# Kernel tuning notes

Measured on AMD Instinct MI355X. Metric: run time of the kernel, lower is better.

Reference implementation:

```python
import jax, jax.numpy as jnp
import numpy as np

DIM = 64  # scaling dim from __init__


def setup_inputs() -> dict:
    key = jax.random.key(0)
    kq, kk, kv = jax.random.split(key, 3)
    B, N, D = 16, 2048, 64
    Q = jax.random.normal(kq, (B, N, D), dtype=jnp.float32)
    K = jax.random.normal(kk, (B, N, D), dtype=jnp.float32)
    V = jax.random.normal(kv, (B, N, D), dtype=jnp.float32)
    return {"Q": Q, "K": K, "V": V}


def reference(Q, K, V):
    # Original transposes K to [B, d, N]; the E/F Linformer projections are
    # constructed but their application guards are always False, so the math
    # is plain scaled-dot-product attention. Dropout p=0 (eval baseline).
    scale = 1.0 / (DIM ** 0.5)
    QK = jnp.einsum('bnd,bmd->bnm', Q, K) * scale          # [B, N, N]
    attn_weights = jax.nn.softmax(QK, axis=-1)             # [B, N, N]
    out = jnp.einsum('bnm,bmd->bnd', attn_weights, V)      # [B, N, d]
    return out, attn_weights
```

## Files before the change

### kernel.cpp

```cpp
#include <hip/hip_runtime.h>

#define B_  16
#define N_  2048
#define D_  64
#define KT  64
#define NTILES (N_ / KT)
#define SCALE_LOG2 0.18033688011112042f

typedef __attribute__((ext_vector_type(8))) short  frag8;
typedef __attribute__((ext_vector_type(4))) float  floatx4;

__device__ __forceinline__ unsigned short f2bf(float f) {
    unsigned int u = __builtin_bit_cast(unsigned int, f);
    u += 0x7fffu + ((u >> 16) & 1u);
    return (unsigned short)(u >> 16);
}

__global__ __launch_bounds__(256) void attn_fused(
    const float* __restrict__ Q, const float* __restrict__ K,
    const float* __restrict__ V, float* __restrict__ out,
    float* __restrict__ attn)
{
    __shared__ unsigned short Qs[64][72];
    __shared__ unsigned short Ks[64][72];
    __shared__ unsigned short Vt[64][72];
    __shared__ unsigned short Ps[4][16][72];

    const int qtile = blockIdx.x;
    const int b     = blockIdx.y;
    const int qbase = qtile * 64;
    const int tid   = threadIdx.x;
    const int w     = tid >> 6;
    const int lane  = tid & 63;
    const int lm    = lane & 15;
    const int quad  = lane >> 4;
    const int q8    = quad * 8;

    const int srow = tid >> 2;
    const int sc0  = (tid & 3) * 16;
    const int vswz = srow ^ (((sc0 >> 4) & 3) << 3);

    {
        const float4* src = (const float4*)(Q + ((size_t)(b*N_ + qbase + srow))*D_ + sc0);
        #pragma unroll
        for (int i = 0; i < 4; ++i) {
            float4 f = src[i];
            ushort4 u; u.x=f2bf(f.x); u.y=f2bf(f.y); u.z=f2bf(f.z); u.w=f2bf(f.w);
            *(ushort4*)&Qs[srow][sc0 + i*4] = u;
        }
    }
    __syncthreads();
    const frag8 aq0 = *(const frag8*)&Qs[w*16 + lm][q8];
    const frag8 aq1 = *(const frag8*)&Qs[w*16 + lm][32 + q8];

    float s[4] = {0.f, 0.f, 0.f, 0.f};

    ushort4 kreg[4];
    {
        const float4* src = (const float4*)(K + ((size_t)(b*N_ + srow))*D_ + sc0);
        #pragma unroll
        for (int i = 0; i < 4; ++i) {
            float4 f = src[i];
            kreg[i].x=f2bf(f.x); kreg[i].y=f2bf(f.y); kreg[i].z=f2bf(f.z); kreg[i].w=f2bf(f.w);
        }
    }

    for (int t = 0; t < NTILES; ++t) {
        __syncthreads();
        #pragma unroll
        for (int i = 0; i < 4; ++i)
            *(ushort4*)&Ks[srow][sc0 + i*4] = kreg[i];
        __syncthreads();

        float4 fnext[4];
        if (t+1 < NTILES) {
            const float4* src = (const float4*)(K + ((size_t)(b*N_ + (t+1)*KT + srow))*D_ + sc0);
            #pragma unroll
            for (int i = 0; i < 4; ++i) fnext[i] = src[i];
        }

        floatx4 acc[4];
        #pragma unroll
        for (int ns = 0; ns < 4; ++ns) {
            frag8 b0 = *(const frag8*)&Ks[ns*16 + lm][q8];
            frag8 b1 = *(const frag8*)&Ks[ns*16 + lm][32 + q8];
            floatx4 a = {0.f, 0.f, 0.f, 0.f};
            a = __builtin_amdgcn_mfma_f32_16x16x32_bf16(aq0, b0, a, 0, 0, 0);
            a = __builtin_amdgcn_mfma_f32_16x16x32_bf16(aq1, b1, a, 0, 0, 0);
            acc[ns] = a;
        }
        #pragma unroll
        for (int ns = 0; ns < 4; ++ns)
            #pragma unroll
            for (int r = 0; r < 4; ++r)
                s[r] += exp2f(acc[ns][r] * SCALE_LOG2);

        if (t+1 < NTILES) {
            #pragma unroll
            for (int i = 0; i < 4; ++i) {
                kreg[i].x=f2bf(fnext[i].x); kreg[i].y=f2bf(fnext[i].y);
                kreg[i].z=f2bf(fnext[i].z); kreg[i].w=f2bf(fnext[i].w);
            }
        }
    }

    float invl[4];
    #pragma unroll
    for (int r = 0; r < 4; ++r) {
        float v = s[r];
        #pragma unroll
        for (int off = 1; off < 16; off <<= 1)
            v += __shfl_xor(v, off, 64);
        invl[r] = 1.0f / v;
    }

    floatx4 oacc[4];
    #pragma unroll
    for (int ns = 0; ns < 4; ++ns) oacc[ns] = (floatx4){0.f, 0.f, 0.f, 0.f};

    unsigned short vbf[16];
    {
        const float4* srcK = (const float4*)(K + ((size_t)(b*N_ + srow))*D_ + sc0);
        const float4* srcV = (const float4*)(V + ((size_t)(b*N_ + srow))*D_ + sc0);
        #pragma unroll
        for (int i = 0; i < 4; ++i) {
            float4 f = srcK[i];
            kreg[i].x=f2bf(f.x); kreg[i].y=f2bf(f.y); kreg[i].z=f2bf(f.z); kreg[i].w=f2bf(f.w);
        }
        #pragma unroll
        for (int i = 0; i < 4; ++i) {
            float4 f = srcV[i];
            vbf[i*4+0]=f2bf(f.x); vbf[i*4+1]=f2bf(f.y);
            vbf[i*4+2]=f2bf(f.z); vbf[i*4+3]=f2bf(f.w);
        }
    }

    for (int t = 0; t < NTILES; ++t) {
        __syncthreads();
        #pragma unroll
        for (int i = 0; i < 4; ++i)
            *(ushort4*)&Ks[srow][sc0 + i*4] = kreg[i];
        #pragma unroll
        for (int i = 0; i < 4; ++i) {
            Vt[sc0 + i*4 + 0][vswz] = vbf[i*4+0];
            Vt[sc0 + i*4 + 1][vswz] = vbf[i*4+1];
            Vt[sc0 + i*4 + 2][vswz] = vbf[i*4+2];
            Vt[sc0 + i*4 + 3][vswz] = vbf[i*4+3];
        }
        __syncthreads();

        float4 fk[4], fv[4];
        if (t+1 < NTILES) {
            const float4* srcK = (const float4*)(K + ((size_t)(b*N_ + (t+1)*KT + srow))*D_ + sc0);
            const float4* srcV = (const float4*)(V + ((size_t)(b*N_ + (t+1)*KT + srow))*D_ + sc0);
            #pragma unroll
            for (int i = 0; i < 4; ++i) fk[i] = srcK[i];
            #pragma unroll
            for (int i = 0; i < 4; ++i) fv[i] = srcV[i];
        }

        floatx4 acc[4];
        #pragma unroll
        for (int ns = 0; ns < 4; ++ns) {
            frag8 b0 = *(const frag8*)&Ks[ns*16 + lm][q8];
            frag8 b1 = *(const frag8*)&Ks[ns*16 + lm][32 + q8];
            floatx4 a = {0.f, 0.f, 0.f, 0.f};
            a = __builtin_amdgcn_mfma_f32_16x16x32_bf16(aq0, b0, a, 0, 0, 0);
            a = __builtin_amdgcn_mfma_f32_16x16x32_bf16(aq1, b1, a, 0, 0, 0);
            acc[ns] = a;
        }

        #pragma unroll
        for (int ns = 0; ns < 4; ++ns) {
            #pragma unroll
            for (int r = 0; r < 4; ++r) {
                float p = exp2f(acc[ns][r] * SCALE_LOG2) * invl[r];
                attn[((size_t)(b*N_ + qbase + w*16 + quad*4 + r))*N_ + t*KT + ns*16 + lm] = p;
                Ps[w][quad*4 + r][ns*16 + lm] = f2bf(p);
            }
        }

        frag8 pa0 = *(const frag8*)&Ps[w][lm][q8];
        frag8 pa1 = *(const frag8*)&Ps[w][lm][32 + q8];
        #pragma unroll
        for (int ns = 0; ns < 4; ++ns) {
            const int kb = q8 ^ (ns << 3);
            frag8 v0 = *(const frag8*)&Vt[ns*16 + lm][kb];
            frag8 v1 = *(const frag8*)&Vt[ns*16 + lm][32 + kb];
            oacc[ns] = __builtin_amdgcn_mfma_f32_16x16x32_bf16(pa0, v0, oacc[ns], 0, 0, 0);
            oacc[ns] = __builtin_amdgcn_mfma_f32_16x16x32_bf16(pa1, v1, oacc[ns], 0, 0, 0);
        }

        if (t+1 < NTILES) {
            #pragma unroll
            for (int i = 0; i < 4; ++i) {
                kreg[i].x=f2bf(fk[i].x); kreg[i].y=f2bf(fk[i].y);
                kreg[i].z=f2bf(fk[i].z); kreg[i].w=f2bf(fk[i].w);
            }
            #pragma unroll
            for (int i = 0; i < 4; ++i) {
                vbf[i*4+0]=f2bf(fv[i].x); vbf[i*4+1]=f2bf(fv[i].y);
                vbf[i*4+2]=f2bf(fv[i].z); vbf[i*4+3]=f2bf(fv[i].w);
            }
        }
    }

    #pragma unroll
    for (int ns = 0; ns < 4; ++ns)
        #pragma unroll
        for (int r = 0; r < 4; ++r)
            out[((size_t)(b*N_ + qbase + w*16 + quad*4 + r))*D_ + ns*16 + lm] = oacc[ns][r];
}

extern "C" void kernel_launch(void* const* d_in, const int* in_sizes, int n_in,
                              void* d_out, int out_size, void* d_ws, size_t ws_size,
                              hipStream_t stream) {
    const float* Q = (const float*)d_in[0];
    const float* K = (const float*)d_in[1];
    const float* V = (const float*)d_in[2];
    float* out  = (float*)d_out;
    float* attn = out + (size_t)B_ * N_ * D_;
    dim3 grid(NTILES, B_);
    attn_fused<<<grid, 256, 0, stream>>>(Q, K, V, out, attn);
}
```

Measured before the change: 419.1 us.

## Stage probabilities in fp32 shared memory for coalesced float4 attn stores

Softmax probabilities are now written to a per-wave fp32 shared buffer and then stored to the attention matrix as row-contiguous float4 writes, replacing scattered scalar global stores. The bf16 P fragments are rebuilt from that buffer. Other changes: Q fragments are loaded straight from global memory without a shared tile, the register prefetch of K/V in the second pass is removed in favour of direct load-then-store each tile, and launch bounds now request 4 blocks per CU. The cost is more shared memory for the fp32 buffer and the loss of global-load overlap in the second loop.

```diff
diff --git a/kernel.cpp b/kernel.cpp
--- a/kernel.cpp
+++ b/kernel.cpp
@@ -10,21 +10,26 @@
 typedef __attribute__((ext_vector_type(8))) short  frag8;
 typedef __attribute__((ext_vector_type(4))) float  floatx4;
 
+union FragU { frag8 fr; unsigned short us[8]; };
+
 __device__ __forceinline__ unsigned short f2bf(float f) {
     unsigned int u = __builtin_bit_cast(unsigned int, f);
     u += 0x7fffu + ((u >> 16) & 1u);
     return (unsigned short)(u >> 16);
 }
 
-__global__ __launch_bounds__(256) void attn_fused(
+struct __align__(16) SMem {
+    unsigned short Ks[64][72];
+    unsigned short Vt[64][72];
+    float          Pf[4][16][68];
+};
+
+__global__ __launch_bounds__(256, 4) void attn_fused(
     const float* __restrict__ Q, const float* __restrict__ K,
     const float* __restrict__ V, float* __restrict__ out,
     float* __restrict__ attn)
 {
-    __shared__ unsigned short Qs[64][72];
-    __shared__ unsigned short Ks[64][72];
-    __shared__ unsigned short Vt[64][72];
-    __shared__ unsigned short Ps[4][16][72];
+    __shared__ SMem sm;
 
     const int qtile = blockIdx.x;
     const int b     = blockIdx.y;
@@ -35,29 +40,31 @@
     const int lm    = lane & 15;
     const int quad  = lane >> 4;
     const int q8    = quad * 8;
+    const size_t bN = (size_t)b * N_;
 
     const int srow = tid >> 2;
     const int sc0  = (tid & 3) * 16;
     const int vswz = srow ^ (((sc0 >> 4) & 3) << 3);
 
+    FragU aq0, aq1;
     {
-        const float4* src = (const float4*)(Q + ((size_t)(b*N_ + qbase + srow))*D_ + sc0);
-        #pragma unroll
-        for (int i = 0; i < 4; ++i) {
-            float4 f = src[i];
-            ushort4 u; u.x=f2bf(f.x); u.y=f2bf(f.y); u.z=f2bf(f.z); u.w=f2bf(f.w);
-            *(ushort4*)&Qs[srow][sc0 + i*4] = u;
-        }
-    }
-    __syncthreads();
-    const frag8 aq0 = *(const frag8*)&Qs[w*16 + lm][q8];
-    const frag8 aq1 = *(const frag8*)&Qs[w*16 + lm][32 + q8];
-
-    float s[4] = {0.f, 0.f, 0.f, 0.f};
+        const float* qp = Q + (bN + qbase + w*16 + lm) * D_;
+        float4 f0 = *(const float4*)(qp + q8);
+        float4 f1 = *(const float4*)(qp + q8 + 4);
+        float4 f2 = *(const float4*)(qp + 32 + q8);
+        float4 f3 = *(const float4*)(qp + 36 + q8);
+        #pragma unroll
+        for (int j = 0; j < 4; ++j) {
+            aq0.us[j]   = f2bf(f0[j]);  aq0.us[4+j] = f2bf(f1[j]);
+            aq1.us[j]   = f2bf(f2[j]);  aq1.us[4+j] = f2bf(f3[j]);
+        }
+    }
+
+    float s4[4] = {0.f, 0.f, 0.f, 0.f};
 
     ushort4 kreg[4];
     {
-        const float4* src = (const float4*)(K + ((size_t)(b*N_ + srow))*D_ + sc0);
+        const float4* src = (const float4*)(K + (bN + srow) * D_ + sc0);
         #pragma unroll
         for (int i = 0; i < 4; ++i) {
             float4 f = src[i];
@@ -69,31 +76,27 @@
         __syncthreads();
         #pragma unroll
         for (int i = 0; i < 4; ++i)
-            *(ushort4*)&Ks[srow][sc0 + i*4] = kreg[i];
+            *(ushort4*)&sm.Ks[srow][sc0 + i*4] = kreg[i];
         __syncthreads();
 
         float4 fnext[4];
         if (t+1 < NTILES) {
-            const float4* src = (const float4*)(K + ((size_t)(b*N_ + (t+1)*KT + srow))*D_ + sc0);
+            const float4* src = (const float4*)(K + (bN + (t+1)*KT + srow) * D_ + sc0);
             #pragma unroll
             for (int i = 0; i < 4; ++i) fnext[i] = src[i];
         }
 
-        floatx4 acc[4];
         #pragma unroll
         for (int ns = 0; ns < 4; ++ns) {
-            frag8 b0 = *(const frag8*)&Ks[ns*16 + lm][q8];
-            frag8 b1 = *(const frag8*)&Ks[ns*16 + lm][32 + q8];
+            frag8 b0 = *(const frag8*)&sm.Ks[ns*16 + lm][q8];
+            frag8 b1 = *(const frag8*)&sm.Ks[ns*16 + lm][32 + q8];
             floatx4 a = {0.f, 0.f, 0.f, 0.f};
-            a = __builtin_amdgcn_mfma_f32_16x16x32_bf16(aq0, b0, a, 0, 0, 0);
-            a = __builtin_amdgcn_mfma_f32_16x16x32_bf16(aq1, b1, a, 0, 0, 0);
-            acc[ns] = a;
-        }
-        #pragma unroll
-        for (int ns = 0; ns < 4; ++ns)
+            a = __builtin_amdgcn_mfma_f32_16x16x32_bf16(aq0.fr, b0, a, 0, 0, 0);
+            a = __builtin_amdgcn_mfma_f32_16x16x32_bf16(aq1.fr, b1, a, 0, 0, 0);
             #pragma unroll
             for (int r = 0; r < 4; ++r)
-                s[r] += exp2f(acc[ns][r] * SCALE_LOG2);
+                s4[r] += exp2f(a[r] * SCALE_LOG2);
+        }
 
         if (t+1 < NTILES) {
             #pragma unroll
@@ -107,7 +110,7 @@
     float invl[4];
     #pragma unroll
     for (int r = 0; r < 4; ++r) {
-        float v = s[r];
+        float v = s4[r];
         #pragma unroll
         for (int off = 1; off < 16; off <<= 1)
             v += __shfl_xor(v, off, 64);
@@ -118,98 +121,90 @@
     #pragma unroll
     for (int ns = 0; ns < 4; ++ns) oacc[ns] = (floatx4){0.f, 0.f, 0.f, 0.f};
 
-    unsigned short vbf[16];
-    {
-        const float4* srcK = (const float4*)(K + ((size_t)(b*N_ + srow))*D_ + sc0);
-        const float4* srcV = (const float4*)(V + ((size_t)(b*N_ + srow))*D_ + sc0);
-        #pragma unroll
-        for (int i = 0; i < 4; ++i) {
-            float4 f = srcK[i];
-            kreg[i].x=f2bf(f.x); kreg[i].y=f2bf(f.y); kreg[i].z=f2bf(f.z); kreg[i].w=f2bf(f.w);
-        }
-        #pragma unroll
-        for (int i = 0; i < 4; ++i) {
-            float4 f = srcV[i];
-            vbf[i*4+0]=f2bf(f.x); vbf[i*4+1]=f2bf(f.y);
-            vbf[i*4+2]=f2bf(f.z); vbf[i*4+3]=f2bf(f.w);
-        }
-    }
+    const int prow = lane >> 3;
+    const int pcol = (lane & 7) * 4;
 
     for (int t = 0; t < NTILES; ++t) {
         __syncthreads();
-        #pragma unroll
-        for (int i = 0; i < 4; ++i)
-            *(ushort4*)&Ks[srow][sc0 + i*4] = kreg[i];
-        #pragma unroll
-        for (int i = 0; i < 4; ++i) {
-            Vt[sc0 + i*4 + 0][vswz] = vbf[i*4+0];
-            Vt[sc0 + i*4 + 1][vswz] = vbf[i*4+1];
-            Vt[sc0 + i*4 + 2][vswz] = vbf[i*4+2];
-            Vt[sc0 + i*4 + 3][vswz] = vbf[i*4+3];
-        }
-        __syncthreads();
-
-        float4 fk[4], fv[4];
-        if (t+1 < NTILES) {
-            const float4* srcK = (const float4*)(K + ((size_t)(b*N_ + (t+1)*KT + srow))*D_ + sc0);
-            const float4* srcV = (const float4*)(V + ((size_t)(b*N_ + (t+1)*KT + srow))*D_ + sc0);
+        {
+            const float4* srcK = (const float4*)(K + (bN + t*KT + srow) * D_ + sc0);
+            const float4* srcV = (const float4*)(V + (bN + t*KT + srow) * D_ + sc0);
+            float4 fk[4], fv[4];
             #pragma unroll
             for (int i = 0; i < 4; ++i) fk[i] = srcK[i];
             #pragma unroll
             for (int i = 0; i < 4; ++i) fv[i] = srcV[i];
-        }
+            #pragma unroll
+            for (int i = 0; i < 4; ++i) {
+                ushort4 u; u.x=f2bf(fk[i].x); u.y=f2bf(fk[i].y);
+                           u.z=f2bf(fk[i].z); u.w=f2bf(fk[i].w);
+                *(ushort4*)&sm.Ks[srow][sc0 + i*4] = u;
+            }
+            #pragma unroll
+            for (int i = 0; i < 4; ++i) {
+                sm.Vt[sc0 + i*4 + 0][vswz] = f2bf(fv[i].x);
+                sm.Vt[sc0 + i*4 + 1][vswz] = f2bf(fv[i].y);
+                sm.Vt[sc0 + i*4 + 2][vswz] = f2bf(fv[i].z);
+                sm.Vt[sc0 + i*4 + 3][vswz] = f2bf(fv[i].w);
+            }
+        }
+        __syncthreads();
 
         floatx4 acc[4];
         #pragma unroll
         for (int ns = 0; ns < 4; ++ns) {
-            frag8 b0 = *(const frag8*)&Ks[ns*16 + lm][q8];
-            frag8 b1 = *(const frag8*)&Ks[ns*16 + lm][32 + q8];
+            frag8 b0 = *(const frag8*)&sm.Ks[ns*16 + lm][q8];
+            frag8 b1 = *(const frag8*)&sm.Ks[ns*16 + lm][32 + q8];
             floatx4 a = {0.f, 0.f, 0.f, 0.f};
-            a = __builtin_amdgcn_mfma_f32_16x16x32_bf16(aq0, b0, a, 0, 0, 0);
-            a = __builtin_amdgcn_mfma_f32_16x16x32_bf16(aq1, b1, a, 0, 0, 0);
+            a = __builtin_amdgcn_mfma_f32_16x16x32_bf16(aq0.fr, b0, a, 0, 0, 0);
+            a = __builtin_amdgcn_mfma_f32_16x16x32_bf16(aq1.fr, b1, a, 0, 0, 0);
             acc[ns] = a;
         }
 
         #pragma unroll
-        for (int ns = 0; ns < 4; ++ns) {
-            #pragma unroll
-            for (int r = 0; r < 4; ++r) {
-                float p = exp2f(acc[ns][r] * SCALE_LOG2) * invl[r];
-                attn[((size_t)(b*N_ + qbase + w*16 + quad*4 + r))*N_ + t*KT + ns*16 + lm] = p;
-                Ps[w][quad*4 + r][ns*16 + lm] = f2bf(p);
-            }
-        }
-
-        frag8 pa0 = *(const frag8*)&Ps[w][lm][q8];
-        frag8 pa1 = *(const frag8*)&Ps[w][lm][32 + q8];
-        #pragma unroll
-        for (int ns = 0; ns < 4; ++ns) {
-            const int kb = q8 ^ (ns << 3);
-            frag8 v0 = *(const frag8*)&Vt[ns*16 + lm][kb];
-            frag8 v1 = *(const frag8*)&Vt[ns*16 + lm][32 + kb];
-            oacc[ns] = __builtin_amdgcn_mfma_f32_16x16x32_bf16(pa0, v0, oacc[ns], 0, 0, 0);
-            oacc[ns] = __builtin_amdgcn_mfma_f32_16x16x32_bf16(pa1, v1, oacc[ns], 0, 0, 0);
-        }
-
-        if (t+1 < NTILES) {
-            #pragma unroll
-            for (int i = 0; i < 4; ++i) {
-                kreg[i].x=f2bf(fk[i].x); kreg[i].y=f2bf(fk[i].y);
-                kreg[i].z=f2bf(fk[i].z); kreg[i].w=f2bf(fk[i].w);
-            }
-            #pragma unroll
-            for (int i = 0; i < 4; ++i) {
-                vbf[i*4+0]=f2bf(fv[i].x); vbf[i*4+1]=f2bf(fv[i].y);
-                vbf[i*4+2]=f2bf(fv[i].z); vbf[i*4+3]=f2bf(fv[i].w);
-            }
+        for (int ns = 0; ns < 4; ++ns)
+            #pragma unroll
+            for (int r = 0; r < 4; ++r)
+                sm.Pf[w][quad*4 + r][ns*16 + lm] =
+                    exp2f(acc[ns][r] * SCALE_LOG2) * invl[r];
+
+        #pragma unroll
+        for (int rg = 0; rg < 2; ++rg)
+            #pragma unroll
+            for (int half = 0; half < 2; ++half) {
+                float4 pv = *(const float4*)&sm.Pf[w][rg*8 + prow][half*32 + pcol];
+                *(float4*)&attn[(bN + qbase + w*16 + rg*8 + prow) * N_
+                                + t*KT + half*32 + pcol] = pv;
+            }
+
+        FragU pa0, pa1;
+        {
+            float4 p0 = *(const float4*)&sm.Pf[w][lm][q8];
+            float4 p1 = *(const float4*)&sm.Pf[w][lm][q8 + 4];
+            float4 p2 = *(const float4*)&sm.Pf[w][lm][32 + q8];
+            float4 p3 = *(const float4*)&sm.Pf[w][lm][36 + q8];
+            #pragma unroll
+            for (int j = 0; j < 4; ++j) {
+                pa0.us[j]   = f2bf(p0[j]);  pa0.us[4+j] = f2bf(p1[j]);
+                pa1.us[j]   = f2bf(p2[j]);  pa1.us[4+j] = f2bf(p3[j]);
+            }
+        }
+
+        #pragma unroll
+        for (int dg = 0; dg < 4; ++dg) {
+            const int kb = q8 ^ (dg << 3);
+            frag8 v0 = *(const frag8*)&sm.Vt[dg*16 + lm][kb];
+            frag8 v1 = *(const frag8*)&sm.Vt[dg*16 + lm][32 + kb];
+            oacc[dg] = __builtin_amdgcn_mfma_f32_16x16x32_bf16(pa0.fr, v0, oacc[dg], 0, 0, 0);
+            oacc[dg] = __builtin_amdgcn_mfma_f32_16x16x32_bf16(pa1.fr, v1, oacc[dg], 0, 0, 0);
         }
     }
 
     #pragma unroll
-    for (int ns = 0; ns < 4; ++ns)
+    for (int dg = 0; dg < 4; ++dg)
         #pragma unroll
         for (int r = 0; r < 4; ++r)
-            out[((size_t)(b*N_ + qbase + w*16 + quad*4 + r))*D_ + ns*16 + lm] = oacc[ns][r];
+            out[(bN + qbase + w*16 + quad*4 + r) * D_ + dg*16 + lm] = oacc[dg][r];
 }
 
 extern "C" void kernel_launch(void* const* d_in, const int* in_sizes, int n_in,
```

After: 375.1 us. 10.5% less time.
